# Kernel optimization log

Measured on AMD Instinct MI355X. Metric: run time of the kernel, lower is better.

## Reference

```python
import jax, jax.numpy as jnp
import numpy as np

N = 1048576   # total nodes
E = 8388608   # total edges
IN = 5        # in_channels
H = 32        # hid_channels
G = 16384     # num graphs
C = 10        # num_classes
L = 2         # conv_unit
EPS = 1e-5


def setup_inputs() -> dict:
    key = jax.random.key(0)
    ks = jax.random.split(key, 16)
    x = jax.random.normal(ks[0], (N, IN), dtype=jnp.float32)
    edge_index = jax.random.randint(ks[1], (2, E), 0, N, dtype=jnp.int64)
    edge_attr = jax.random.uniform(ks[2], (E, 1), dtype=jnp.float32)
    batch = jnp.sort(jax.random.randint(ks[3], (N,), 0, G, dtype=jnp.int64))
    s_in = 1.0 / np.sqrt(IN)
    s_h = 1.0 / np.sqrt(H)
    s_2h = 1.0 / np.sqrt(2 * H)
    W_emb = jax.random.normal(ks[4], (H, IN), dtype=jnp.float32) * s_in
    b_emb = jnp.zeros((H,), dtype=jnp.float32)
    W_rel = jax.random.normal(ks[5], (L, H, H), dtype=jnp.float32) * s_h
    b_rel = jnp.zeros((L, H), dtype=jnp.float32)
    W_root = jax.random.normal(ks[6], (L, H, H), dtype=jnp.float32) * s_h
    bn_gamma = jnp.ones((L, H), dtype=jnp.float32)
    bn_beta = jnp.zeros((L, H), dtype=jnp.float32)
    W1 = jax.random.normal(ks[7], (2 * H, H), dtype=jnp.float32) * s_h
    b1 = jnp.zeros((2 * H,), dtype=jnp.float32)
    W2 = jax.random.normal(ks[8], (C, 2 * H), dtype=jnp.float32) * s_2h
    b2 = jnp.zeros((C,), dtype=jnp.float32)
    return {
        "x": x, "edge_index": edge_index, "edge_attr": edge_attr, "batch": batch,
        "W_emb": W_emb, "b_emb": b_emb, "W_rel": W_rel, "b_rel": b_rel,
        "W_root": W_root, "bn_gamma": bn_gamma, "bn_beta": bn_beta,
        "W1": W1, "b1": b1, "W2": W2, "b2": b2,
    }


def _graph_conv(x, src, dst, ew, Wrel, brel, Wroot):
    # PyG GraphConv: lin_rel(scatter_add(ew * x[src] -> dst)) + lin_root(x)
    msg = x[src] * ew[:, None]                              # [E, H]
    agg = jax.ops.segment_sum(msg, dst, num_segments=N)     # [N, H]
    return agg @ Wrel.T + brel + x @ Wroot.T


def _batch_norm(x, gamma, beta):
    mean = jnp.mean(x, axis=0)
    var = jnp.mean(jnp.square(x - mean), axis=0)  # biased, as torch training BN
    return (x - mean) * jax.lax.rsqrt(var + EPS) * gamma + beta


def reference(x, edge_index, edge_attr, batch, W_emb, b_emb, W_rel, b_rel,
              W_root, bn_gamma, bn_beta, W1, b1, W2, b2):
    src, dst = edge_index[0], edge_index[1]
    ew = edge_attr.reshape(-1)
    h = x @ W_emb.T + b_emb                                  # node_emb
    for i in range(L):
        h = _graph_conv(h, src, dst, ew, W_rel[i], b_rel[i], W_root[i])
        h = jax.nn.relu(_batch_norm(h, bn_gamma[i], bn_beta[i]))
    graph_x = jax.ops.segment_max(h, batch, num_segments=G)  # global_max_pool
    hidden = jax.nn.relu(graph_x @ W1.T + b1)
    return hidden @ W2.T + b2                                # [G, C]
```

## Files before the change

### kernel.cpp

```cpp
#include <hip/hip_runtime.h>
#include <hip/hip_fp16.h>

#define NN 1048576
#define NE 8388608
#define NG 16384
#define NBUCK 256
#define BSH 12
#define EPB (NE / 256)

typedef _Float16 half8 __attribute__((ext_vector_type(8)));
typedef float f32x16 __attribute__((ext_vector_type(16)));

__global__ __launch_bounds__(256) void k_embed(const float* __restrict__ x,
    const float* __restrict__ W, const float* __restrict__ b, __half* __restrict__ h) {
  __shared__ float sW[160];
  __shared__ float sb[32];
  int t = threadIdx.x;
  if (t < 160) sW[t] = W[t];
  if (t < 32) sb[t] = b[t];
  __syncthreads();
  int idx = blockIdx.x * 256 + t;
  int c = idx & 31, n = idx >> 5;
  const float* xr = x + n * 5;
  float acc = sb[c];
#pragma unroll
  for (int k = 0; k < 5; ++k) acc = fmaf(xr[k], sW[c * 5 + k], acc);
  h[idx] = __float2half(acc);
}

__global__ __launch_bounds__(256) void k_pcnt(const int* __restrict__ dst, int* __restrict__ hist) {
  __shared__ int lh[NBUCK];
  int t = threadIdx.x;
  lh[t] = 0;
  __syncthreads();
  int base = blockIdx.x * EPB;
  for (int e = base + t; e < base + EPB; e += 256)
    atomicAdd(&lh[dst[e] >> BSH], 1);
  __syncthreads();
  hist[t * 256 + blockIdx.x] = lh[t];
}

__global__ __launch_bounds__(256) void k_scanA(int* __restrict__ hist, int* __restrict__ tot) {
  __shared__ int s2[256];
  int b = blockIdx.x, t = threadIdx.x;
  int v = hist[b * 256 + t];
  s2[t] = v; __syncthreads();
  for (int st = 1; st < 256; st <<= 1) {
    int a = (t >= st) ? s2[t - st] : 0; __syncthreads(); s2[t] += a; __syncthreads();
  }
  hist[b * 256 + t] = s2[t] - v;
  if (t == 255) tot[b] = s2[255];
}

__global__ __launch_bounds__(256) void k_scanB(const int* __restrict__ tot, int* __restrict__ gbase) {
  __shared__ int s2[256];
  int t = threadIdx.x;
  int c = tot[t];
  s2[t] = c; __syncthreads();
  for (int st = 1; st < 256; st <<= 1) {
    int a = (t >= st) ? s2[t - st] : 0; __syncthreads(); s2[t] += a; __syncthreads();
  }
  gbase[t] = s2[t] - c;
  if (t == 255) gbase[256] = s2[255];
}

__global__ __launch_bounds__(256) void k_part(const int* __restrict__ ei, const float* __restrict__ ew,
                                              const int* __restrict__ hist, const int* __restrict__ gbase,
                                              uint2* __restrict__ bsw, int* __restrict__ bdd) {
  __shared__ int cur[NBUCK];
  int t = threadIdx.x, blk = blockIdx.x;
  cur[t] = gbase[t] + hist[t * 256 + blk];
  __syncthreads();
  int base = blk * EPB;
  for (int e = base + t; e < base + EPB; e += 256) {
    int src = ei[e];
    int d   = ei[NE + e];
    unsigned wb = __float_as_uint(ew[e]);
    int b = d >> BSH;
    int pos = atomicAdd(&cur[b], 1);
    bsw[pos] = make_uint2((unsigned)src, wb);
    bdd[pos] = d;
  }
}

__global__ __launch_bounds__(256) void k_fillD(const int* __restrict__ gbase, const uint2* __restrict__ bsw,
                                               const int* __restrict__ bdd, int* __restrict__ rowptr,
                                               uint2* __restrict__ colw) {
  __shared__ int loc[4096];
  __shared__ int s2[256];
  int t = threadIdx.x, b = blockIdx.x;
  int beg = gbase[b], end = gbase[b + 1], gb = beg;
  int node_base = b << BSH;
#pragma unroll
  for (int j = 0; j < 16; ++j) loc[t * 16 + j] = 0;
  __syncthreads();
  for (int i = beg + t; i < end; i += 256) atomicAdd(&loc[bdd[i] & 4095], 1);
  __syncthreads();
  int v[16]; int tsum = 0;
#pragma unroll
  for (int j = 0; j < 16; ++j) { v[j] = loc[t * 16 + j]; tsum += v[j]; }
  s2[t] = tsum; __syncthreads();
  for (int st = 1; st < 256; st <<= 1) {
    int a = (t >= st) ? s2[t - st] : 0; __syncthreads(); s2[t] += a; __syncthreads();
  }
  int run = s2[t] - tsum;
#pragma unroll
  for (int j = 0; j < 16; ++j) {
    loc[t * 16 + j] = run;
    rowptr[node_base + t * 16 + j] = gb + run;
    run += v[j];
  }
  if (b == NBUCK - 1 && t == 255) rowptr[NN] = NE;
  __syncthreads();
  for (int i = beg + t; i < end; i += 256) {
    int d = bdd[i];
    int p = atomicAdd(&loc[d & 4095], 1);
    colw[gb + p] = bsw[i];
  }
}

__global__ __launch_bounds__(256) void k_gbound(const int* __restrict__ batch, int* __restrict__ gptr) {
  int n = blockIdx.x * 256 + threadIdx.x;
  int b = batch[n];
  int prev = (n == 0) ? -1 : batch[n - 1];
  for (int g = prev + 1; g <= b; ++g) gptr[g] = n;
  if (n == NN - 1) {
    for (int g = b + 1; g <= NG; ++g) gptr[g] = NN;
  }
}

__global__ __launch_bounds__(256) void k_agglin(
    const int* __restrict__ rowptr, const uint2* __restrict__ colw,
    const __half* __restrict__ hIn, const float* __restrict__ Wrel,
    const float* __restrict__ brel, const float* __restrict__ Wroot,
    __half* __restrict__ hPre, double* __restrict__ stats) {
  __shared__ __half sA[4][1024];
  __shared__ uint2 sE[256];
  __shared__ double rS[256], rQ[256];
  int t = threadIdx.x;
  int wv = t >> 6, lane = t & 63;
  int c = lane & 31, hi = lane >> 5, grp = t >> 5;
  char* myA = (char*)sA[wv];

  half8 bfr[4];
#pragma unroll
  for (int m = 0; m < 4; ++m)
#pragma unroll
    for (int j = 0; j < 8; ++j) {
      int k = 16 * m + hi * 8 + j;
      float w = (k < 32) ? Wrel[c * 32 + k] : Wroot[c * 32 + (k - 32)];
      bfr[m][j] = (_Float16)w;
    }
  float bias = brel[c];
  double aS = 0.0, aQ = 0.0;

  for (int tile = blockIdx.x * 4 + wv; tile < NN / 32; tile += gridDim.x * 4) {
    int nbase = tile * 32;
    for (int r = 0; r < 16; ++r) {
      int node = 2 * r + hi;
      int n = nbase + node;
      int r0 = rowptr[n], r1 = rowptr[n + 1];
      float acc = 0.f;
      for (int j = r0; j < r1; j += 32) {
        int m_ = r1 - j; if (m_ > 32) m_ = 32;
        uint2 cw = make_uint2(0u, 0u);
        if (c < m_) cw = colw[j + c];
        sE[t] = cw;
        int mm = (m_ + 7) & ~7;
        for (int i = 0; i < mm; i += 8) {
          const uint4* eb4 = (const uint4*)&sE[grp * 32 + i];
          uint4 q0 = eb4[0], q1 = eb4[1], q2 = eb4[2], q3 = eb4[3];
          float h0 = __half2float(hIn[(size_t)q0.x * 32 + c]);
          float h1 = __half2float(hIn[(size_t)q0.z * 32 + c]);
          float h2 = __half2float(hIn[(size_t)q1.x * 32 + c]);
          float h3 = __half2float(hIn[(size_t)q1.z * 32 + c]);
          float h4 = __half2float(hIn[(size_t)q2.x * 32 + c]);
          float h5 = __half2float(hIn[(size_t)q2.z * 32 + c]);
          float h6 = __half2float(hIn[(size_t)q3.x * 32 + c]);
          float h7 = __half2float(hIn[(size_t)q3.z * 32 + c]);
          acc = fmaf(__uint_as_float(q0.y), h0, acc);
          acc = fmaf(__uint_as_float(q0.w), h1, acc);
          acc = fmaf(__uint_as_float(q1.y), h2, acc);
          acc = fmaf(__uint_as_float(q1.w), h3, acc);
          acc = fmaf(__uint_as_float(q2.y), h4, acc);
          acc = fmaf(__uint_as_float(q2.w), h5, acc);
          acc = fmaf(__uint_as_float(q3.y), h6, acc);
          acc = fmaf(__uint_as_float(q3.w), h7, acc);
        }
      }
      int bw = (node * 64 + c * 2) ^ ((node & 7) << 4);
      *(__half*)(myA + bw) = __float2half(acc);
    }
    f32x16 d;
#pragma unroll
    for (int r = 0; r < 16; ++r) d[r] = bias;
#pragma unroll
    for (int m = 0; m < 4; ++m) {
      half8 a;
      if (m < 2) {
        int node = c;
        int br = (node * 64 + (16 * m + hi * 8) * 2) ^ ((node & 7) << 4);
        a = *(const half8*)(myA + br);
      } else {
        int node = c;
        int chb = 16 * (m - 2) + hi * 8;
        a = *(const half8*)(hIn + (size_t)(nbase + node) * 32 + chb);
      }
      d = __builtin_amdgcn_mfma_f32_32x32x16_f16(a, bfr[m], d, 0, 0, 0);
    }
#pragma unroll
    for (int r = 0; r < 16; ++r) {
      int node = (r & 3) + 8 * (r >> 2) + 4 * hi;
      float v = d[r];
      hPre[(size_t)(nbase + node) * 32 + c] = __float2half(v);
      aS += v; aQ += (double)v * v;
    }
  }
  rS[t] = aS; rQ[t] = aQ;
  __syncthreads();
  for (int s = 128; s >= 32; s >>= 1) {
    if (t < s) { rS[t] += rS[t + s]; rQ[t] += rQ[t + s]; }
    __syncthreads();
  }
  if (t < 32) {
    atomicAdd(&stats[t], rS[t]);
    atomicAdd(&stats[32 + t], rQ[t]);
  }
}

__global__ void k_bnfin(const double* __restrict__ stats, const float* __restrict__ gamma,
                        const float* __restrict__ beta, float* __restrict__ ss) {
  int c = threadIdx.x;
  double mean = stats[c] * (1.0 / NN);
  double var = stats[32 + c] * (1.0 / NN) - mean * mean;
  float scale = gamma[c] * (float)(1.0 / sqrt(var + 1e-5));
  ss[c] = scale;
  ss[32 + c] = beta[c] - (float)mean * scale;
}

__global__ __launch_bounds__(256) void k_apply(const __half* __restrict__ in,
    const float* __restrict__ ss, __half* __restrict__ outp) {
  __shared__ float s0[32], s1[32];
  int t = threadIdx.x;
  if (t < 32) { s0[t] = ss[t]; s1[t] = ss[32 + t]; }
  __syncthreads();
  int idx = blockIdx.x * 256 + t;
  int c = idx & 31;
  float v = fmaxf(fmaf(__half2float(in[idx]), s0[c], s1[c]), 0.f);
  outp[idx] = __float2half(v);
}

__global__ __launch_bounds__(256) void k_pool(const __half* __restrict__ hB,
    const float* __restrict__ ss, const int* __restrict__ gptr, float* __restrict__ pooled) {
  __shared__ float s0[32], s1[32];
  int t = threadIdx.x;
  if (t < 32) { s0[t] = ss[t]; s1[t] = ss[32 + t]; }
  __syncthreads();
  int wv = t >> 6, lane = t & 63;
  int c = lane & 31, p = lane >> 5;
  int g = blockIdx.x * 4 + wv;
  int a = gptr[g], b = gptr[g + 1];
  float mx = 0.f;
  for (int n = a + p; n < b; n += 2)
    mx = fmaxf(mx, fmaf(__half2float(hB[(size_t)n * 32 + c]), s0[c], s1[c]));
  mx = fmaxf(mx, __shfl_xor(mx, 32, 64));
  if (p == 0) pooled[g * 32 + c] = mx;
}

__global__ __launch_bounds__(256) void k_head(const float* __restrict__ pooled,
    const float* __restrict__ W1, const float* __restrict__ b1,
    const float* __restrict__ W2, const float* __restrict__ b2, float* __restrict__ out) {
  __shared__ float sW1[64 * 33], sW2[10 * 65], sb1[64], sb2[10];
  __shared__ float sHid[4][64];
  int t = threadIdx.x;
  for (int i = t; i < 2048; i += 256) sW1[(i >> 5) * 33 + (i & 31)] = W1[i];
  for (int i = t; i < 640; i += 256) sW2[(i >> 6) * 65 + (i & 63)] = W2[i];
  if (t < 64) sb1[t] = b1[t];
  if (t < 10) sb2[t] = b2[t];
  __syncthreads();
  int w = t >> 6, lane = t & 63;
  for (int g = blockIdx.x * 4 + w; g < NG; g += gridDim.x * 4) {
    float pv = (lane < 32) ? pooled[g * 32 + lane] : 0.f;
    float acc = sb1[lane];
#pragma unroll
    for (int k = 0; k < 32; ++k)
      acc = fmaf(__shfl(pv, k, 64), sW1[lane * 33 + k], acc);
    acc = fmaxf(acc, 0.f);
    sHid[w][lane] = acc;
    __syncthreads();
    if (lane < 10) {
      float o = sb2[lane];
#pragma unroll
      for (int j = 0; j < 64; ++j) o = fmaf(sHid[w][j], sW2[lane * 65 + j], o);
      out[g * 10 + lane] = o;
    }
    __syncthreads();
  }
}

extern "C" void kernel_launch(void* const* d_in, const int* in_sizes, int n_in,
                              void* d_out, int out_size, void* d_ws, size_t ws_size,
                              hipStream_t stream) {
  const float* x      = (const float*)d_in[0];
  const int*   ei     = (const int*)d_in[1];
  const float* ea     = (const float*)d_in[2];
  const int*   batch  = (const int*)d_in[3];
  const float* W_emb  = (const float*)d_in[4];
  const float* b_emb  = (const float*)d_in[5];
  const float* W_rel  = (const float*)d_in[6];
  const float* b_rel  = (const float*)d_in[7];
  const float* W_root = (const float*)d_in[8];
  const float* gamma  = (const float*)d_in[9];
  const float* beta   = (const float*)d_in[10];
  const float* W1     = (const float*)d_in[11];
  const float* b1     = (const float*)d_in[12];
  const float* W2     = (const float*)d_in[13];
  const float* b2     = (const float*)d_in[14];
  float* out = (float*)d_out;

  char* ws = (char*)d_ws;
  size_t off = 0;
  __half* hA    = (__half*)(ws + off); off += (size_t)NN * 32 * 2;
  uint2*  colw  = (uint2*)(ws + off);  off += (size_t)NE * 8;
  uint2*  bsw   = (uint2*)(ws + off);
  __half* hB    = (__half*)(ws + off);
  off += (size_t)NE * 8;
  int*    bdd   = (int*)(ws + off);    off += (size_t)NE * 4;
  int*    rowptr= (int*)(ws + off);    off += ((size_t)NN + 64) * 4;
  int*    hist  = (int*)(ws + off);    off += (size_t)NBUCK * 256 * 4;
  int*    tot   = (int*)(ws + off);    off += 1024;
  int*    gbase = (int*)(ws + off);    off += 2048;
  int*    gptr  = (int*)(ws + off);    off += ((size_t)NG + 64) * 4;
  float*  pooled= (float*)(ws + off);
  double* stats = (double*)d_out;
  float*  ss    = (float*)((char*)d_out + 512);

  k_embed<<<NN * 32 / 256, 256, 0, stream>>>(x, W_emb, b_emb, hA);

  k_pcnt <<<256, 256, 0, stream>>>(ei + NE, hist);
  k_scanA<<<NBUCK, 256, 0, stream>>>(hist, tot);
  k_scanB<<<1, 256, 0, stream>>>(tot, gbase);
  k_part <<<256, 256, 0, stream>>>(ei, ea, hist, gbase, bsw, bdd);
  k_fillD<<<NBUCK, 256, 0, stream>>>(gbase, bsw, bdd, rowptr, colw);
  k_gbound<<<NN / 256, 256, 0, stream>>>(batch, gptr);

  for (int l = 0; l < 2; ++l) {
    (void)hipMemsetAsync(stats, 0, 64 * 8, stream);
    k_agglin<<<2048, 256, 0, stream>>>(rowptr, colw, hA, W_rel + l * 1024,
                                       b_rel + l * 32, W_root + l * 1024, hB, stats);
    k_bnfin<<<1, 32, 0, stream>>>(stats, gamma + l * 32, beta + l * 32, ss);
    if (l == 0) {
      k_apply<<<NN * 32 / 256, 256, 0, stream>>>(hB, ss, hA);
    } else {
      k_pool<<<NG / 4, 256, 0, stream>>>(hB, ss, gptr, pooled);
    }
  }
  k_head<<<1024, 256, 0, stream>>>(pooled, W1, b1, W2, b2, out);
}
```

Measured before the change: 1.128 ms.

## Fuse layer-1 BN+ReLU into second aggregation, pack dst into src, vectorize gathers

Removes the separate BN-apply pass by applying scale/shift+ReLU to gathered neighbor and root features inside the second aggregation kernel, ping-ponging buffers hA/hB. Packs the low 12 bits of dst into the src word during partitioning, dropping the separate bdd array and its traffic. Gathers now load half2 per lane with two edges processed in parallel per wave and combined via shuffle, and pooling uses half2 loads. Risks: BN is recomputed per edge gather (more ALU), src<<12 assumes src fits in 20 bits (N=2^20 holds).

After: 1.012 ms. 1.11x faster.

```diff
diff --git a/kernel.cpp b/kernel.cpp
--- a/kernel.cpp
+++ b/kernel.cpp
@@ -66,7 +66,7 @@
 
 __global__ __launch_bounds__(256) void k_part(const int* __restrict__ ei, const float* __restrict__ ew,
                                               const int* __restrict__ hist, const int* __restrict__ gbase,
-                                              uint2* __restrict__ bsw, int* __restrict__ bdd) {
+                                              uint2* __restrict__ bsw) {
   __shared__ int cur[NBUCK];
   int t = threadIdx.x, blk = blockIdx.x;
   cur[t] = gbase[t] + hist[t * 256 + blk];
@@ -78,14 +78,12 @@
     unsigned wb = __float_as_uint(ew[e]);
     int b = d >> BSH;
     int pos = atomicAdd(&cur[b], 1);
-    bsw[pos] = make_uint2((unsigned)src, wb);
-    bdd[pos] = d;
+    bsw[pos] = make_uint2(((unsigned)src << 12) | (unsigned)(d & 4095), wb);
   }
 }
 
 __global__ __launch_bounds__(256) void k_fillD(const int* __restrict__ gbase, const uint2* __restrict__ bsw,
-                                               const int* __restrict__ bdd, int* __restrict__ rowptr,
-                                               uint2* __restrict__ colw) {
+                                               int* __restrict__ rowptr, uint2* __restrict__ colw) {
   __shared__ int loc[4096];
   __shared__ int s2[256];
   int t = threadIdx.x, b = blockIdx.x;
@@ -94,7 +92,7 @@
 #pragma unroll
   for (int j = 0; j < 16; ++j) loc[t * 16 + j] = 0;
   __syncthreads();
-  for (int i = beg + t; i < end; i += 256) atomicAdd(&loc[bdd[i] & 4095], 1);
+  for (int i = beg + t; i < end; i += 256) atomicAdd(&loc[bsw[i].x & 4095], 1);
   __syncthreads();
   int v[16]; int tsum = 0;
 #pragma unroll
@@ -113,9 +111,9 @@
   if (b == NBUCK - 1 && t == 255) rowptr[NN] = NE;
   __syncthreads();
   for (int i = beg + t; i < end; i += 256) {
-    int d = bdd[i];
-    int p = atomicAdd(&loc[d & 4095], 1);
-    colw[gb + p] = bsw[i];
+    uint2 r = bsw[i];
+    int p = atomicAdd(&loc[r.x & 4095], 1);
+    colw[gb + p] = make_uint2(r.x >> 12, r.y);
   }
 }
 
@@ -129,18 +127,31 @@
   }
 }
 
+template <int FUSE_BN>
 __global__ __launch_bounds__(256) void k_agglin(
     const int* __restrict__ rowptr, const uint2* __restrict__ colw,
-    const __half* __restrict__ hIn, const float* __restrict__ Wrel,
-    const float* __restrict__ brel, const float* __restrict__ Wroot,
-    __half* __restrict__ hPre, double* __restrict__ stats) {
+    const __half* __restrict__ hIn, const float* __restrict__ bnss,
+    const float* __restrict__ Wrel, const float* __restrict__ brel,
+    const float* __restrict__ Wroot, __half* __restrict__ hPre,
+    double* __restrict__ stats) {
   __shared__ __half sA[4][1024];
   __shared__ uint2 sE[256];
+  __shared__ float sBn[64];
   __shared__ double rS[256], rQ[256];
   int t = threadIdx.x;
   int wv = t >> 6, lane = t & 63;
   int c = lane & 31, hi = lane >> 5, grp = t >> 5;
+  int slot = (lane >> 4) & 1, cl = lane & 15;
   char* myA = (char*)sA[wv];
+
+  if (FUSE_BN && t < 64) sBn[t] = bnss[t];
+  __syncthreads();
+
+  float bs0x = 0.f, bs0y = 0.f, bs1x = 0.f, bs1y = 0.f;
+  if constexpr (FUSE_BN) {
+    bs0x = bnss[2 * cl];      bs0y = bnss[2 * cl + 1];
+    bs1x = bnss[32 + 2 * cl]; bs1y = bnss[32 + 2 * cl + 1];
+  }
 
   half8 bfr[4];
 #pragma unroll
@@ -160,7 +171,7 @@
       int node = 2 * r + hi;
       int n = nbase + node;
       int r0 = rowptr[n], r1 = rowptr[n + 1];
-      float acc = 0.f;
+      float2 acc = make_float2(0.f, 0.f);
       for (int j = r0; j < r1; j += 32) {
         int m_ = r1 - j; if (m_ > 32) m_ = 32;
         uint2 cw = make_uint2(0u, 0u);
@@ -168,28 +179,27 @@
         sE[t] = cw;
         int mm = (m_ + 7) & ~7;
         for (int i = 0; i < mm; i += 8) {
-          const uint4* eb4 = (const uint4*)&sE[grp * 32 + i];
-          uint4 q0 = eb4[0], q1 = eb4[1], q2 = eb4[2], q3 = eb4[3];
-          float h0 = __half2float(hIn[(size_t)q0.x * 32 + c]);
-          float h1 = __half2float(hIn[(size_t)q0.z * 32 + c]);
-          float h2 = __half2float(hIn[(size_t)q1.x * 32 + c]);
-          float h3 = __half2float(hIn[(size_t)q1.z * 32 + c]);
-          float h4 = __half2float(hIn[(size_t)q2.x * 32 + c]);
-          float h5 = __half2float(hIn[(size_t)q2.z * 32 + c]);
-          float h6 = __half2float(hIn[(size_t)q3.x * 32 + c]);
-          float h7 = __half2float(hIn[(size_t)q3.z * 32 + c]);
-          acc = fmaf(__uint_as_float(q0.y), h0, acc);
-          acc = fmaf(__uint_as_float(q0.w), h1, acc);
-          acc = fmaf(__uint_as_float(q1.y), h2, acc);
-          acc = fmaf(__uint_as_float(q1.w), h3, acc);
-          acc = fmaf(__uint_as_float(q2.y), h4, acc);
-          acc = fmaf(__uint_as_float(q2.w), h5, acc);
-          acc = fmaf(__uint_as_float(q3.y), h6, acc);
-          acc = fmaf(__uint_as_float(q3.w), h7, acc);
+#pragma unroll
+          for (int k = 0; k < 4; ++k) {
+            uint2 e = sE[grp * 32 + i + 2 * k + slot];
+            __half2 hv2 = *(const __half2*)(hIn + (size_t)(e.x) * 32 + 2 * cl);
+            float w = __uint_as_float(e.y);
+            float2 hf = __half22float2(hv2);
+            if constexpr (FUSE_BN) {
+              hf.x = fmaxf(fmaf(hf.x, bs0x, bs1x), 0.f);
+              hf.y = fmaxf(fmaf(hf.y, bs0y, bs1y), 0.f);
+            }
+            acc.x = fmaf(w, hf.x, acc.x);
+            acc.y = fmaf(w, hf.y, acc.y);
+          }
         }
       }
-      int bw = (node * 64 + c * 2) ^ ((node & 7) << 4);
-      *(__half*)(myA + bw) = __float2half(acc);
+      acc.x += __shfl_xor(acc.x, 16, 64);
+      acc.y += __shfl_xor(acc.y, 16, 64);
+      if (slot == 0) {
+        int bw = (node * 64 + cl * 4) ^ ((node & 7) << 4);
+        *(__half2*)(myA + bw) = __float22half2_rn(acc);
+      }
     }
     f32x16 d;
 #pragma unroll
@@ -202,9 +212,16 @@
         int br = (node * 64 + (16 * m + hi * 8) * 2) ^ ((node & 7) << 4);
         a = *(const half8*)(myA + br);
       } else {
-        int node = c;
         int chb = 16 * (m - 2) + hi * 8;
-        a = *(const half8*)(hIn + (size_t)(nbase + node) * 32 + chb);
+        a = *(const half8*)(hIn + (size_t)(nbase + c) * 32 + chb);
+        if constexpr (FUSE_BN) {
+#pragma unroll
+          for (int j = 0; j < 8; ++j) {
+            float v = (float)a[j];
+            v = fmaxf(fmaf(v, sBn[chb + j], sBn[32 + chb + j]), 0.f);
+            a[j] = (_Float16)v;
+          }
+        }
       }
       d = __builtin_amdgcn_mfma_f32_32x32x16_f16(a, bfr[m], d, 0, 0, 0);
     }
@@ -238,33 +255,24 @@
   ss[32 + c] = beta[c] - (float)mean * scale;
 }
 
-__global__ __launch_bounds__(256) void k_apply(const __half* __restrict__ in,
-    const float* __restrict__ ss, __half* __restrict__ outp) {
-  __shared__ float s0[32], s1[32];
-  int t = threadIdx.x;
-  if (t < 32) { s0[t] = ss[t]; s1[t] = ss[32 + t]; }
-  __syncthreads();
-  int idx = blockIdx.x * 256 + t;
-  int c = idx & 31;
-  float v = fmaxf(fmaf(__half2float(in[idx]), s0[c], s1[c]), 0.f);
-  outp[idx] = __float2half(v);
-}
-
 __global__ __launch_bounds__(256) void k_pool(const __half* __restrict__ hB,
     const float* __restrict__ ss, const int* __restrict__ gptr, float* __restrict__ pooled) {
-  __shared__ float s0[32], s1[32];
-  int t = threadIdx.x;
-  if (t < 32) { s0[t] = ss[t]; s1[t] = ss[32 + t]; }
-  __syncthreads();
+  int t = threadIdx.x;
   int wv = t >> 6, lane = t & 63;
-  int c = lane & 31, p = lane >> 5;
+  int p = lane >> 4, cl = lane & 15;
+  float s0x = ss[2 * cl], s0y = ss[2 * cl + 1];
+  float s1x = ss[32 + 2 * cl], s1y = ss[32 + 2 * cl + 1];
   int g = blockIdx.x * 4 + wv;
   int a = gptr[g], b = gptr[g + 1];
-  float mx = 0.f;
-  for (int n = a + p; n < b; n += 2)
-    mx = fmaxf(mx, fmaf(__half2float(hB[(size_t)n * 32 + c]), s0[c], s1[c]));
-  mx = fmaxf(mx, __shfl_xor(mx, 32, 64));
-  if (p == 0) pooled[g * 32 + c] = mx;
+  float mx = 0.f, my = 0.f;
+  for (int n = a + p; n < b; n += 4) {
+    float2 hv = __half22float2(*(const __half2*)(hB + (size_t)n * 32 + 2 * cl));
+    mx = fmaxf(mx, fmaf(hv.x, s0x, s1x));
+    my = fmaxf(my, fmaf(hv.y, s0y, s1y));
+  }
+  mx = fmaxf(mx, __shfl_xor(mx, 16, 64)); my = fmaxf(my, __shfl_xor(my, 16, 64));
+  mx = fmaxf(mx, __shfl_xor(mx, 32, 64)); my = fmaxf(my, __shfl_xor(my, 32, 64));
+  if (p == 0) *(float2*)&pooled[g * 32 + 2 * cl] = make_float2(mx, my);
 }
 
 __global__ __launch_bounds__(256) void k_head(const float* __restrict__ pooled,
@@ -325,7 +333,6 @@
   uint2*  bsw   = (uint2*)(ws + off);
   __half* hB    = (__half*)(ws + off);
   off += (size_t)NE * 8;
-  int*    bdd   = (int*)(ws + off);    off += (size_t)NE * 4;
   int*    rowptr= (int*)(ws + off);    off += ((size_t)NN + 64) * 4;
   int*    hist  = (int*)(ws + off);    off += (size_t)NBUCK * 256 * 4;
   int*    tot   = (int*)(ws + off);    off += 1024;
@@ -333,27 +340,28 @@
   int*    gptr  = (int*)(ws + off);    off += ((size_t)NG + 64) * 4;
   float*  pooled= (float*)(ws + off);
   double* stats = (double*)d_out;
-  float*  ss    = (float*)((char*)d_out + 512);
+  float*  ss0   = (float*)((char*)d_out + 512);
+  float*  ss1   = (float*)((char*)d_out + 768);
 
   k_embed<<<NN * 32 / 256, 256, 0, stream>>>(x, W_emb, b_emb, hA);
 
   k_pcnt <<<256, 256, 0, stream>>>(ei + NE, hist);
   k_scanA<<<NBUCK, 256, 0, stream>>>(hist, tot);
   k_scanB<<<1, 256, 0, stream>>>(tot, gbase);
-  k_part <<<256, 256, 0, stream>>>(ei, ea, hist, gbase, bsw, bdd);
-  k_fillD<<<NBUCK, 256, 0, stream>>>(gbase, bsw, bdd, rowptr, colw);
+  k_part <<<256, 256, 0, stream>>>(ei, ea, hist, gbase, bsw);
+  k_fillD<<<NBUCK, 256, 0, stream>>>(gbase, bsw, rowptr, colw);
   k_gbound<<<NN / 256, 256, 0, stream>>>(batch, gptr);
 
-  for (int l = 0; l < 2; ++l) {
-    (void)hipMemsetAsync(stats, 0, 64 * 8, stream);
-    k_agglin<<<2048, 256, 0, stream>>>(rowptr, colw, hA, W_rel + l * 1024,
-                                       b_rel + l * 32, W_root + l * 1024, hB, stats);
-    k_bnfin<<<1, 32, 0, stream>>>(stats, gamma + l * 32, beta + l * 32, ss);
-    if (l == 0) {
-      k_apply<<<NN * 32 / 256, 256, 0, stream>>>(hB, ss, hA);
-    } else {
-      k_pool<<<NG / 4, 256, 0, stream>>>(hB, ss, gptr, pooled);
-    }
-  }
+  (void)hipMemsetAsync(stats, 0, 64 * 8, stream);
+  k_agglin<0><<<2048, 256, 0, stream>>>(rowptr, colw, hA, nullptr,
+                                        W_rel, b_rel, W_root, hB, stats);
+  k_bnfin<<<1, 32, 0, stream>>>(stats, gamma, beta, ss0);
+
+  (void)hipMemsetAsync(stats, 0, 64 * 8, stream);
+  k_agglin<1><<<2048, 256, 0, stream>>>(rowptr, colw, hB, ss0,
+                                        W_rel + 1024, b_rel + 32, W_root + 1024, hA, stats);
+  k_bnfin<<<1, 32, 0, stream>>>(stats, gamma + 32, beta + 32, ss1);
+
+  k_pool<<<NG / 4, 256, 0, stream>>>(hA, ss1, gptr, pooled);
   k_head<<<1024, 256, 0, stream>>>(pooled, W1, b1, W2, b2, out);
 }
```
